# Kernel tuning notes

Hardware: AMD Instinct MI355X
Metric: run time of the kernel (lower is better)

The kernel has to match this reference:

```python
import jax, jax.numpy as jnp
import numpy as np
from jax import lax

B, IN_CH, H, W = 512, 20, 32, 32
FEAT, NUM_AGENTS, NUM_ACTIONS = 128, 4, 16
NUM_UNIT, NUM_CITY = 12, 4


def setup_inputs() -> dict:
    key = jax.random.key(0)
    ks = jax.random.split(key, 6)
    states = jax.random.normal(ks[0], (B, IN_CH, H, W), dtype=jnp.float32)
    labels = jax.random.randint(ks[1], (B,), 0, NUM_AGENTS, dtype=jnp.int32)
    maskings = jnp.ones((B, 1, H, W), dtype=jnp.float32)
    # get_feature params: 3x3 conv trunk (stand-in for PolicyNetwork.get_feature)
    conv_w = jax.random.normal(ks[2], (FEAT, IN_CH, 3, 3), dtype=jnp.float32) * 0.05
    conv_b = jnp.zeros((FEAT,), dtype=jnp.float32)
    # Stacked per-agent heads: index 0 = policy_net.fc1, 1.. = fc_list
    W_all = jax.random.normal(ks[3], (NUM_AGENTS, NUM_ACTIONS, FEAT), dtype=jnp.float32) * 0.05
    b_all = jax.random.normal(ks[4], (NUM_AGENTS, NUM_ACTIONS), dtype=jnp.float32) * 0.05
    return {"states": states, "labels": labels, "maskings": maskings,
            "conv_w": conv_w, "conv_b": conv_b, "W_all": W_all, "b_all": b_all}


def _get_feature(states, maskings, conv_w, conv_b):
    x = lax.conv_general_dilated(states, conv_w, (1, 1), 'SAME',
                                 dimension_numbers=('NCHW', 'OIHW', 'NCHW'))
    x = jax.nn.relu(x + conv_b[None, :, None, None])
    return x * maskings  # [B, FEAT, H, W]


def reference(states, labels, maskings, conv_w, conv_b, W_all, b_all):
    x = _get_feature(states, maskings, conv_w, conv_b)
    b, c, h, w = x.shape
    x = x.transpose(0, 2, 3, 1).reshape(b, h * w, c)  # [B, HW, C]
    # Equivalent to computing all num_agents heads then gathering by label:
    # select each sample's head weights, then one batched GEMM.
    W_sel = W_all[labels]          # [B, K, C]
    b_sel = b_all[labels]          # [B, K]
    out = jnp.einsum('bnc,bkc->bnk', x, W_sel) + b_sel[:, None, :]
    out = out.reshape(b, h, w, NUM_ACTIONS)
    return out[..., :NUM_UNIT], out[..., NUM_UNIT:]
```

## Files before the change

### kernel.cpp

```cpp
#include <hip/hip_runtime.h>
#include <hip/hip_bf16.h>
#include <stdint.h>

#define BATCH   512
#define INCH    20
#define FEAT    128
#define KACT    16
#define NUNIT   12

typedef short bf16x8 __attribute__((ext_vector_type(8)));
typedef float f32x4  __attribute__((ext_vector_type(4)));

#define BPACK_ELEMS (3*2*4*128*8)
#define WHEAD_ELEMS (4*4*4*16*8)

#define XIN_ELEMS   (34*34*20 + 64)

__device__ __forceinline__ uint16_t f2bf(float f) {
    union { float f; uint32_t u; } x{f};
    uint32_t u = x.u;
    return (uint16_t)((u + 0x7FFFu + ((u >> 16) & 1u)) >> 16);
}

__device__ __forceinline__ uint32_t cvt_pk_bf16(float lo, float hi) {
    uint32_t r;
    asm("v_cvt_pk_bf16_f32 %0, %1, %2" : "=v"(r) : "v"(lo), "v"(hi));
    return r;
}

__global__ void repack_kernel(const float* __restrict__ conv_w,
                              const float* __restrict__ W_all,
                              uint16_t* __restrict__ Bpack,
                              uint16_t* __restrict__ Whead) {
    int idx = blockIdx.x * 256 + threadIdx.x;
    if (idx < BPACK_ELEMS) {
        int j = idx & 7, t = idx >> 3;
        int f = t & 127; t >>= 7;
        int g = t & 3;   t >>= 2;
        int kk = t & 1;  int ky = t >> 1;
        int k = kk * 32 + g * 8 + j;
        float v = 0.0f;
        if (k < 60) {
            int kx = k / 20, c = k % 20;
            v = conv_w[((f * INCH + c) * 3 + ky) * 3 + kx];
        }
        Bpack[idx] = f2bf(v);
    } else if (idx < BPACK_ELEMS + WHEAD_ELEMS) {
        int i = idx - BPACK_ELEMS;
        int j = i & 7, t = i >> 3;
        int a = t & 15; t >>= 4;
        int g = t & 3;  t >>= 2;
        int kt = t & 3; int ag = t >> 2;
        int f = kt * 32 + g * 8 + j;
        Whead[i] = f2bf(W_all[(ag * KACT + a) * FEAT + f]);
    }
}

__global__ __launch_bounds__(512, 4) void fused_mfma_kernel(
    const float* __restrict__ states,
    const int*   __restrict__ labels,
    const float* __restrict__ maskings,
    const float* __restrict__ conv_b,
    const float* __restrict__ b_all,
    const uint16_t* __restrict__ Bpack,
    const uint16_t* __restrict__ Whead,
    float*       __restrict__ out)
{
    __shared__ __align__(16) uint16_t xin[XIN_ELEMS];
    __shared__ __align__(16) uint16_t xl[2 * 64 * 128];

    const int b    = blockIdx.x;
    const int tid  = threadIdx.x;
    const int lane = tid & 63;
    const int w    = tid >> 6;
    const int l15  = lane & 15;
    const int g    = lane >> 4;
    const int wr   = w >> 2;
    const int fq   = w & 3;
    const int swz  = (l15 & 7) << 4;

    for (int i = tid; i < XIN_ELEMS / 8; i += 512)
        ((uint4*)xin)[i] = uint4{0, 0, 0, 0};
    __syncthreads();

    for (int t = 0; t < 10; ++t) {
        int i  = t * 512 + tid;
        int p  = i & 1023;
        int cg = i >> 10;
        int y  = p >> 5, x = p & 31;
        const float* sp = states + (size_t)b * (INCH * 1024) + cg * 4096 + p;
        float v0 = sp[0], v1 = sp[1024], v2 = sp[2048], v3 = sp[3072];
        uint64_t lo = cvt_pk_bf16(v0, v1);
        uint64_t hi = cvt_pk_bf16(v2, v3);
        *(uint64_t*)&xin[((y + 1) * 34 + (x + 1)) * 20 + cg * 4] = lo | (hi << 32);
    }

    const int label = labels[b];
    f32x4 cb[2];
    #pragma unroll
    for (int nt = 0; nt < 2; ++nt)
        cb[nt] = *(const f32x4*)&conv_b[fq * 32 + nt * 16 + g * 4];
    const f32x4 hb = *(const f32x4*)&b_all[label * KACT + g * 4];
    bf16x8 Wh[4];
    #pragma unroll
    for (int kt = 0; kt < 4; ++kt)
        Wh[kt] = *(const bf16x8*)&Whead[(((label * 4 + kt) * 4 + g) * 16 + l15) * 8];

    bf16x8 Wc[3][2][2];
    #pragma unroll
    for (int ky = 0; ky < 3; ++ky)
        #pragma unroll
        for (int kk = 0; kk < 2; ++kk)
            #pragma unroll
            for (int nt = 0; nt < 2; ++nt)
                Wc[ky][kk][nt] = *(const bf16x8*)
                    &Bpack[((((ky * 2 + kk) * 4 + g) * 128 + fq * 32 + nt * 16 + l15) * 8)];

    __syncthreads();

    #pragma unroll 2
    for (int s = 0; s < 16; ++s) {
        const int y = s * 2 + wr;

        const float m0 = maskings[(size_t)b * 1024 + y * 32 + l15];
        const float m1 = maskings[(size_t)b * 1024 + y * 32 + 16 + l15];

        f32x4 acc[2][2];
        #pragma unroll
        for (int pt = 0; pt < 2; ++pt)
            #pragma unroll
            for (int nt = 0; nt < 2; ++nt)
                acc[pt][nt] = f32x4{0.f, 0.f, 0.f, 0.f};

        #pragma unroll
        for (int ky = 0; ky < 3; ++ky) {
            const uint64_t* a0 = (const uint64_t*)&xin[((y + ky) * 34 + l15) * 20 + g * 8];
            const uint64_t* a1 = (const uint64_t*)&xin[((y + ky) * 34 + 16 + l15) * 20 + g * 8];
            #pragma unroll
            for (int kk = 0; kk < 2; ++kk) {
                union { uint64_t u[2]; bf16x8 v; } B0, B1;
                B0.u[0] = a0[kk * 8 + 0]; B0.u[1] = a0[kk * 8 + 1];
                B1.u[0] = a1[kk * 8 + 0]; B1.u[1] = a1[kk * 8 + 1];
                #pragma unroll
                for (int nt = 0; nt < 2; ++nt) {
                    acc[0][nt] = __builtin_amdgcn_mfma_f32_16x16x32_bf16(
                        Wc[ky][kk][nt], B0.v, acc[0][nt], 0, 0, 0);
                    acc[1][nt] = __builtin_amdgcn_mfma_f32_16x16x32_bf16(
                        Wc[ky][kk][nt], B1.v, acc[1][nt], 0, 0, 0);
                }
            }
        }

        char* xbase = (char*)xl + (s & 1) * 16384;
        #pragma unroll
        for (int pt = 0; pt < 2; ++pt) {
            const float m = pt ? m1 : m0;
            #pragma unroll
            for (int nt = 0; nt < 2; ++nt) {
                float x0 = fmaxf(acc[pt][nt][0] + cb[nt][0], 0.f) * m;
                float x1 = fmaxf(acc[pt][nt][1] + cb[nt][1], 0.f) * m;
                float x2 = fmaxf(acc[pt][nt][2] + cb[nt][2], 0.f) * m;
                float x3 = fmaxf(acc[pt][nt][3] + cb[nt][3], 0.f) * m;
                uint64_t pk = (uint64_t)cvt_pk_bf16(x0, x1)
                            | ((uint64_t)cvt_pk_bf16(x2, x3) << 32);
                const int off = ((wr * 2 + pt) * 16 + l15) * 256 + fq * 64 + nt * 32 + g * 8;
                *(uint64_t*)(xbase + (off ^ swz)) = pk;
            }
        }

        __syncthreads();

        if (fq < 2) {
            f32x4 hacc = f32x4{0.f, 0.f, 0.f, 0.f};
            #pragma unroll
            for (int kt = 0; kt < 4; ++kt) {
                const int off = ((wr * 2 + fq) * 16 + l15) * 256 + kt * 64 + g * 16;
                bf16x8 bx = *(const bf16x8*)(xbase + (off ^ swz));
                hacc = __builtin_amdgcn_mfma_f32_16x16x32_bf16(Wh[kt], bx, hacc, 0, 0, 0);
            }
            const size_t pos = (size_t)b * 1024 + y * 32 + fq * 16 + l15;
            f32x4 o = hacc + hb;
            if (g < 3) *(f32x4*)&out[pos * NUNIT + g * 4] = o;
            else       *(f32x4*)&out[(size_t)BATCH * 1024 * NUNIT + pos * 4] = o;
        }
    }
}

extern "C" void kernel_launch(void* const* d_in, const int* in_sizes, int n_in,
                              void* d_out, int out_size, void* d_ws, size_t ws_size,
                              hipStream_t stream) {
    const float* states   = (const float*)d_in[0];
    const int*   labels   = (const int*)d_in[1];
    const float* maskings = (const float*)d_in[2];
    const float* conv_w   = (const float*)d_in[3];
    const float* conv_b   = (const float*)d_in[4];
    const float* W_all    = (const float*)d_in[5];
    const float* b_all    = (const float*)d_in[6];
    float* out = (float*)d_out;

    uint16_t* Bpack = (uint16_t*)d_ws;
    uint16_t* Whead = Bpack + BPACK_ELEMS;

    repack_kernel<<<(BPACK_ELEMS + WHEAD_ELEMS + 255) / 256, 256, 0, stream>>>(
        conv_w, W_all, Bpack, Whead);
    fused_mfma_kernel<<<BATCH, 512, 0, stream>>>(
        states, labels, maskings, conv_b, b_all, Bpack, Whead, out);
}
```

Baseline: 43.59 us.

## Software-pipeline head GEMM one row behind conv and raise MFMA priority

The per-row head GEMM now runs one iteration late: its LDS operands from the previous row's double buffer are loaded before the conv MFMAs, and its MFMAs and stores follow them. The last row is handled in an epilogue after the loop. The aim is to hide LDS latency and the fq<2 imbalance behind conv work. Wave priority is raised around the MFMA blocks. The cost is more registers for the prefetched head operands and extra epilogue code.

Measured after the change: 59.18 us. +35.8%, slower.

```diff
diff --git a/kernel.cpp b/kernel.cpp
--- a/kernel.cpp
+++ b/kernel.cpp
@@ -116,6 +116,9 @@
                 Wc[ky][kk][nt] = *(const bf16x8*)
                     &Bpack[((((ky * 2 + kk) * 4 + g) * 128 + fq * 32 + nt * 16 + l15) * 8)];
 
+    const int hoff0 = ((wr * 2 + fq) * 16 + l15) * 256;
+    const bool do_head = (fq < 2);
+
     __syncthreads();
 
     #pragma unroll 2
@@ -125,6 +128,14 @@
         const float m0 = maskings[(size_t)b * 1024 + y * 32 + l15];
         const float m1 = maskings[(size_t)b * 1024 + y * 32 + 16 + l15];
 
+        bf16x8 hx[4];
+        char* hrd = (char*)xl + ((s + 1) & 1) * 16384;
+        if (do_head && s > 0) {
+            #pragma unroll
+            for (int kt = 0; kt < 4; ++kt)
+                hx[kt] = *(const bf16x8*)(hrd + ((hoff0 + kt * 64 + g * 16) ^ swz));
+        }
+
         f32x4 acc[2][2];
         #pragma unroll
         for (int pt = 0; pt < 2; ++pt)
@@ -132,6 +143,7 @@
             for (int nt = 0; nt < 2; ++nt)
                 acc[pt][nt] = f32x4{0.f, 0.f, 0.f, 0.f};
 
+        __builtin_amdgcn_s_setprio(1);
         #pragma unroll
         for (int ky = 0; ky < 3; ++ky) {
             const uint64_t* a0 = (const uint64_t*)&xin[((y + ky) * 34 + l15) * 20 + g * 8];
@@ -150,6 +162,20 @@
                 }
             }
         }
+        __builtin_amdgcn_s_setprio(0);
+
+        if (do_head && s > 0) {
+            f32x4 hacc = f32x4{0.f, 0.f, 0.f, 0.f};
+            __builtin_amdgcn_s_setprio(1);
+            #pragma unroll
+            for (int kt = 0; kt < 4; ++kt)
+                hacc = __builtin_amdgcn_mfma_f32_16x16x32_bf16(Wh[kt], hx[kt], hacc, 0, 0, 0);
+            __builtin_amdgcn_s_setprio(0);
+            const size_t pos = (size_t)b * 1024 + ((s - 1) * 2 + wr) * 32 + fq * 16 + l15;
+            f32x4 o = hacc + hb;
+            if (g < 3) *(f32x4*)&out[pos * NUNIT + g * 4] = o;
+            else       *(f32x4*)&out[(size_t)BATCH * 1024 * NUNIT + pos * 4] = o;
+        }
 
         char* xbase = (char*)xl + (s & 1) * 16384;
         #pragma unroll
@@ -169,20 +195,20 @@
         }
 
         __syncthreads();
-
-        if (fq < 2) {
-            f32x4 hacc = f32x4{0.f, 0.f, 0.f, 0.f};
-            #pragma unroll
-            for (int kt = 0; kt < 4; ++kt) {
-                const int off = ((wr * 2 + fq) * 16 + l15) * 256 + kt * 64 + g * 16;
-                bf16x8 bx = *(const bf16x8*)(xbase + (off ^ swz));
-                hacc = __builtin_amdgcn_mfma_f32_16x16x32_bf16(Wh[kt], bx, hacc, 0, 0, 0);
-            }
-            const size_t pos = (size_t)b * 1024 + y * 32 + fq * 16 + l15;
-            f32x4 o = hacc + hb;
-            if (g < 3) *(f32x4*)&out[pos * NUNIT + g * 4] = o;
-            else       *(f32x4*)&out[(size_t)BATCH * 1024 * NUNIT + pos * 4] = o;
-        }
+    }
+
+    if (do_head) {
+        char* hrd = (char*)xl + 16384;
+        f32x4 hacc = f32x4{0.f, 0.f, 0.f, 0.f};
+        #pragma unroll
+        for (int kt = 0; kt < 4; ++kt) {
+            bf16x8 hx = *(const bf16x8*)(hrd + ((hoff0 + kt * 64 + g * 16) ^ swz));
+            hacc = __builtin_amdgcn_mfma_f32_16x16x32_bf16(Wh[kt], hx, hacc, 0, 0, 0);
+        }
+        const size_t pos = (size_t)b * 1024 + (30 + wr) * 32 + fq * 16 + l15;
+        f32x4 o = hacc + hb;
+        if (g < 3) *(f32x4*)&out[pos * NUNIT + g * 4] = o;
+        else       *(f32x4*)&out[(size_t)BATCH * 1024 * NUNIT + pos * 4] = o;
     }
 }
 
```
